# Optimization experiments

Measured on AMD Instinct MI355X. Metric: run time of the kernel, lower is better.

Reference implementation:

```python
import jax, jax.numpy as jnp
import numpy as np

R, C, H, W = 500, 512, 38, 38      # rois, VGG channels, feature-map HxW (img 608 / 16)
K, HID, POOL, SCALE = 20, 4096, 3, 16
FEAT = C * POOL * POOL             # 4608, matches fc6 in_features


def setup_inputs():
    key = jax.random.key(0)
    ks = jax.random.split(key, 12)
    fmap = jax.random.normal(ks[0], (C, H, W), dtype=jnp.float32)
    # ROIs in original image coords (x1,y1,x2,y2); width/height >= 48 px so that
    # after /16 + floor every ROI is non-degenerate (none filtered out).
    x1 = jax.random.randint(ks[1], (R,), 0, 288)
    y1 = jax.random.randint(ks[2], (R,), 0, 288)
    bw = jax.random.randint(ks[3], (R,), 48, 304)
    bh = jax.random.randint(ks[4], (R,), 48, 304)
    rois = jnp.stack([x1, y1, x1 + bw, y1 + bh], axis=1).astype(jnp.float32)
    label = jax.random.bernoulli(ks[5], 0.3, (K,)).astype(jnp.float32)
    s = 0.01
    W6 = jax.random.normal(ks[6], (FEAT, HID), jnp.float32) * s
    b6 = jnp.zeros((HID,), jnp.float32)
    W7 = jax.random.normal(ks[7], (HID, HID), jnp.float32) * s
    b7 = jnp.zeros((HID,), jnp.float32)
    W8c = jax.random.normal(ks[8], (HID, K), jnp.float32) * s
    b8c = jnp.zeros((K,), jnp.float32)
    W8d = jax.random.normal(ks[9], (HID, K), jnp.float32) * s
    b8d = jnp.zeros((K,), jnp.float32)
    return dict(fmap=fmap, rois=rois, label=label, W6=W6, b6=b6, W7=W7, b7=b7,
                W8c=W8c, b8c=b8c, W8d=W8d, b8d=b8d)


def _roi_pool(fmap, rois):
    # scaled_rois = origin_rois / 16, sliced as integer indices (floor)
    sc = jnp.floor(rois / SCALE).astype(jnp.int32)          # [R,4]
    x1, y1, x2, y2 = sc[:, 0], sc[:, 1], sc[:, 2], sc[:, 3]

    def binmask(lo, hi, size):
        # adaptive-max-pool bins: [lo + floor(j*L/3), lo + ceil((j+1)*L/3))
        L = hi - lo                                          # [R]
        j = jnp.arange(POOL)
        start = lo[:, None] + (j[None, :] * L[:, None]) // POOL
        end = lo[:, None] + (-((-(j[None, :] + 1) * L[:, None]) // POOL))
        pos = jnp.arange(size)
        return (pos[None, None, :] >= start[:, :, None]) & (pos[None, None, :] < end[:, :, None])

    cm = binmask(x1, x2, W)                                  # [R,3,W]
    rm = binmask(y1, y2, H)                                  # [R,3,H]
    neg = jnp.finfo(fmap.dtype).min
    # max over x within each x-bin: [R,C,H,3]
    tmp = jnp.max(jnp.where(cm[:, None, None, :, :], fmap[None, :, :, None, :], neg), axis=-1)
    # max over y within each y-bin: [R,C,3,3]
    pooled = jnp.max(jnp.where(rm[:, None, :, :, None], tmp[:, :, None, :, :], neg), axis=3)
    return pooled.reshape(R, FEAT), sc.astype(jnp.float32)


def _spatial_reg(scores, fc7, rois_sc, label):
    # faithful to original: argsort ascending, index 0 taken as the reference box,
    # and bboxes_iou interprets (x1,y1,x2,y2) as (x,y,w,h) — replicated as-is.
    idx = jnp.argsort(scores, axis=0)                        # [R,K]

    def per_class(idx_k, s_k, lab_k):
        h, rest = idx_k[0], idx_k[1:]
        hb = rois_sc[h]                                      # [4]
        rb = rois_sc[rest]                                   # [R-1,4]
        b1x2, b1y2 = rb[:, 0] + rb[:, 2], rb[:, 1] + rb[:, 3]
        b2x2, b2y2 = hb[0] + hb[2], hb[1] + hb[3]
        iw = jnp.clip(jnp.minimum(b1x2, b2x2) - jnp.maximum(rb[:, 0], hb[0]) + 1, 0)
        ih = jnp.clip(jnp.minimum(b1y2, b2y2) - jnp.maximum(rb[:, 1], hb[1]) + 1, 0)
        inter = iw * ih
        a1 = (b1x2 - rb[:, 0] + 1) * (b1y2 - rb[:, 1] + 1)
        a2 = (b2x2 - hb[0] + 1) * (b2y2 - hb[1] + 1)
        iou = inter / (a1 + a2 - inter)
        m = (iou > 0.6).astype(fc7.dtype)                    # [R-1]
        rf = fc7[rest] * m[:, None]
        diff = (rf - fc7[h]) * s_k[rest][:, None]
        return lab_k * 0.5 * jnp.sum(diff * diff)

    regs = jax.vmap(per_class)(idx.T, scores.T, label)       # [K]
    return jnp.sum(regs) / K


def reference(fmap, rois, label, W6, b6, W7, b7, W8c, b8c, W8d, b8d):
    feat, rois_sc = _roi_pool(fmap, rois)                    # [R,4608]
    fc6 = feat @ W6 + b6
    fc7 = fc6 @ W7 + b7
    pc = jax.nn.softmax(fc7 @ W8c + b8c, axis=1)             # per-roi over classes
    pd = jax.nn.softmax(fc7 @ W8d + b8d, axis=0)             # per-class over rois
    scores = pc * pd                                         # [R,K]
    out = jnp.sum(scores, axis=0)                            # [K], in (0,1)
    bce = -jnp.mean(label * jnp.log(out) + (1.0 - label) * jnp.log(1.0 - out))
    reg = _spatial_reg(scores, fc7, rois_sc, label)
    return scores, bce + reg, reg
```

## Files before the change

kernel.cpp:

```cpp
#include <hip/hip_runtime.h>
#include <cstdint>
#include <cstddef>

#define DEV __device__ __forceinline__

typedef __bf16 bf16_t;
typedef __bf16 bf16x8 __attribute__((ext_vector_type(8)));
typedef float  f32x4  __attribute__((ext_vector_type(4)));
typedef float  f32x2  __attribute__((ext_vector_type(2)));
typedef unsigned int u32x4 __attribute__((ext_vector_type(4)));

DEV bf16_t f2bf(float x) { return (bf16_t)x; }

constexpr int R_ = 500, C_ = 512, H_ = 38, W_ = 38, K_ = 20;
constexpr int HID = 4096, FEAT = 4608, MP = 512;
constexpr int HW = H_ * W_;
constexpr int KSPLIT = 4;

constexpr size_t alup(size_t x) { return (x + 255) & ~(size_t)255; }
constexpr size_t O_FMT  = 0;
constexpr size_t O_RSC  = alup(O_FMT  + (size_t)HW*C_*4);
constexpr size_t O_FEAT = alup(O_RSC  + (size_t)R_*4*4);
constexpr size_t O_FC6  = alup(O_FEAT + (size_t)MP*FEAT*2);
constexpr size_t O_FC7  = alup(O_FC6  + (size_t)MP*HID*2);
constexpr size_t O_PC   = alup(O_FC7  + (size_t)MP*HID*4);
constexpr size_t O_LD   = alup(O_PC   + (size_t)R_*K_*4);
constexpr size_t O_AN   = alup(O_LD   + (size_t)R_*K_*4);
constexpr size_t O_OS   = alup(O_AN   + (size_t)MP*4);
constexpr size_t O_HI   = alup(O_OS   + (size_t)K_*4);
constexpr size_t O_D    = alup(O_HI   + (size_t)K_*4);
constexpr size_t O_W8T  = alup(O_D    + (size_t)R_*K_*4);
constexpr size_t O_W7T  = alup(O_W8T  + (size_t)2*K_*HID*4);
constexpr size_t O_PART = alup(O_W7T  + (size_t)HID*HID*2);
constexpr size_t O_HP   = O_PART;
constexpr size_t O_DP   = O_PART + (size_t)4*1024*1024;

__global__ void __launch_bounds__(256) k_prep(const float* __restrict__ fmap,
                                              float* __restrict__ fmapt,
                                              const float* __restrict__ W8c,
                                              const float* __restrict__ W8d,
                                              float* __restrict__ W8T,
                                              const float* __restrict__ W7,
                                              bf16_t* __restrict__ W7T) {
    int b = blockIdx.x, t = threadIdx.x;
    if (b < 736) {
        __shared__ float tile[32][33];
        int p0 = (b % 46) * 32, c0 = (b / 46) * 32;
        int tx = t & 31, ty = t >> 5;
#pragma unroll
        for (int i = 0; i < 4; ++i) {
            int c = c0 + ty + i*8, p = p0 + tx;
            tile[ty + i*8][tx] = (p < HW) ? fmap[(size_t)c*HW + p] : 0.f;
        }
        __syncthreads();
#pragma unroll
        for (int i = 0; i < 4; ++i) {
            int p = p0 + ty + i*8, c = c0 + tx;
            if (p < HW) fmapt[(size_t)p*C_ + c] = tile[tx][ty + i*8];
        }
    } else if (b < 776) {
        int k = b - 736;
        const float* src = (k < K_) ? W8c : W8d;
        int kk = (k < K_) ? k : k - K_;
        for (int i = t; i < HID; i += 256)
            W8T[(size_t)k*HID + i] = src[(size_t)i*K_ + kk];
    } else {
        __shared__ float tile[64][65];
        int j = b - 776;
        int k0 = (j >> 6) * 64, n0 = (j & 63) * 64;
#pragma unroll
        for (int i = 0; i < 16; ++i) {
            int idx = t + i*256;
            int kk = idx >> 6, nn = idx & 63;
            tile[kk][nn] = W7[(size_t)(k0 + kk)*HID + n0 + nn];
        }
        __syncthreads();
#pragma unroll
        for (int i = 0; i < 8; ++i) {
            int idx = t + i*256;
            int nn = idx >> 5, kw = idx & 31;
            bf16_t a = f2bf(tile[2*kw][nn]), c = f2bf(tile[2*kw + 1][nn]);
            unsigned int u = ((unsigned short*)&a)[0] | ((unsigned int)((unsigned short*)&c)[0] << 16);
            *reinterpret_cast<unsigned int*>(&W7T[(size_t)(n0 + nn)*HID + k0 + 2*kw]) = u;
        }
    }
}

__global__ void __launch_bounds__(256) k_roipool(const float* __restrict__ fmapt,
                                                 const float* __restrict__ rois,
                                                 bf16_t* __restrict__ feat,
                                                 float* __restrict__ rois_sc) {
    int r = blockIdx.x, bin = blockIdx.y, t = threadIdx.x;
    if (r >= R_) {
        feat[(size_t)r*FEAT + (size_t)t*9       + bin] = (bf16_t)0.f;
        feat[(size_t)r*FEAT + (size_t)(t+256)*9 + bin] = (bf16_t)0.f;
        return;
    }
    int x1 = (int)floorf(rois[r*4+0] * 0.0625f);
    int y1 = (int)floorf(rois[r*4+1] * 0.0625f);
    int x2 = (int)floorf(rois[r*4+2] * 0.0625f);
    int y2 = (int)floorf(rois[r*4+3] * 0.0625f);
    if (bin == 0 && t == 0) {
        rois_sc[r*4+0] = (float)x1; rois_sc[r*4+1] = (float)y1;
        rois_sc[r*4+2] = (float)x2; rois_sc[r*4+3] = (float)y2;
    }
    int Lx = x2 - x1, Ly = y2 - y1;
    int pr = bin / 3, px = bin - pr*3;
    int rs = y1 + (pr*Ly)/3, re = y1 + ((pr+1)*Ly + 2)/3;
    int cs = x1 + (px*Lx)/3, ce = x1 + ((px+1)*Lx + 2)/3;
    float m0 = -3.402823466e38f, m1 = -3.402823466e38f;
    for (int y = rs; y < re; ++y) {
        const float* rowp = fmapt + (size_t)(y*W_)*C_;
        for (int x = cs; x < ce; ++x) {
            const float* p = rowp + (size_t)x*C_;
            m0 = fmaxf(m0, p[t]);
            m1 = fmaxf(m1, p[t + 256]);
        }
    }
    feat[(size_t)r*FEAT + (size_t)t*9       + bin] = f2bf(m0);
    feat[(size_t)r*FEAT + (size_t)(t+256)*9 + bin] = f2bf(m1);
}

__global__ void __launch_bounds__(512, 4)
k_gemm(const bf16_t* __restrict__ A, const float* __restrict__ B,
       float* __restrict__ part, int KDIM, int nts) {
    __shared__ bf16_t Asm[2][128*64];
    __shared__ bf16_t Bsm[2][128*64];
    const int t = threadIdx.x;
    const int lane = t & 63, wid = t >> 6;
    const int wr = wid >> 2, wc = wid & 3;

    const int flat = blockIdx.x + 32*blockIdx.y + 128*blockIdx.z;
    const int q = 16 * gridDim.z;
    const int v = (flat & 7) * q + (flat >> 3);
    const int by = v & 3, bx = (v >> 2) & 31, bz = v >> 7;

    const int brow = by * 128, bcol = bx * 128;
    const int kt0 = bz * nts;

    f32x4 acc[4][2] = {};
    f32x2 br[8];
    const int n2 = t & 63, kgl = t >> 6;

    auto stage_A = [&](int kt, int buf) {
        const bf16_t* Ag = A + (size_t)brow*KDIM + kt*64;
#pragma unroll
        for (int i = 0; i < 2; ++i) {
            int s = t + i*512;
            int row = s >> 3;
            int kb = (s & 7) ^ ((row >> 1) & 7);
            const bf16_t* src = Ag + (size_t)row*KDIM + kb*8;
            bf16_t* dst = &Asm[buf][(size_t)(i*512 + (t & ~63)) * 8];
            __builtin_amdgcn_global_load_lds(
                (const __attribute__((address_space(1))) void*)src,
                (__attribute__((address_space(3))) void*)dst, 16, 0, 0);
        }
    };
    auto load_B = [&](int kt) {
        const float* src = B + (size_t)(kt*64 + kgl*8)*HID + bcol + 2*n2;
#pragma unroll
        for (int j = 0; j < 8; ++j)
            br[j] = *reinterpret_cast<const f32x2*>(src + (size_t)j*HID);
    };
    auto write_B = [&](int buf) {
        const int sw = n2 & 7;
        bf16x8 v0, v1;
#pragma unroll
        for (int j = 0; j < 8; ++j) { v0[j] = f2bf(br[j].x); v1[j] = f2bf(br[j].y); }
        *reinterpret_cast<u32x4*>(&Bsm[buf][(size_t)((2*n2    )*8 + (kgl ^ sw)) * 8]) = *reinterpret_cast<u32x4*>(&v0);
        *reinterpret_cast<u32x4*>(&Bsm[buf][(size_t)((2*n2 + 1)*8 + (kgl ^ sw)) * 8]) = *reinterpret_cast<u32x4*>(&v1);
    };

    stage_A(kt0, 0);
    load_B(kt0);
    write_B(0);
    __syncthreads();

    for (int it = 0; it < nts; ++it) {
        const int cur = it & 1;
        if (it + 1 < nts) { stage_A(kt0 + it + 1, cur ^ 1); load_B(kt0 + it + 1); }
#pragma unroll
        for (int kk = 0; kk < 2; ++kk) {
            const int kb = kk*4 + (lane >> 4);
            bf16x8 af[4], bfr[2];
#pragma unroll
            for (int m = 0; m < 4; ++m) {
                int row = wr*64 + m*16 + (lane & 15);
                af[m] = *reinterpret_cast<const bf16x8*>(
                    &Asm[cur][(size_t)(row*8 + (kb ^ ((row >> 1) & 7))) * 8]);
            }
#pragma unroll
            for (int n = 0; n < 2; ++n) {
                int nn = wc*32 + n*16 + (lane & 15);
                bfr[n] = *reinterpret_cast<const bf16x8*>(
                    &Bsm[cur][(size_t)(nn*8 + (kb ^ ((nn >> 1) & 7))) * 8]);
            }
#pragma unroll
            for (int m = 0; m < 4; ++m)
#pragma unroll
                for (int n = 0; n < 2; ++n)
                    acc[m][n] = __builtin_amdgcn_mfma_f32_16x16x32_bf16(af[m], bfr[n], acc[m][n], 0, 0, 0);
        }
        if (it + 1 < nts) { write_B(cur ^ 1); __syncthreads(); }
    }

    float* dst = part + (size_t)bz * MP * HID;
#pragma unroll
    for (int m = 0; m < 4; ++m) {
        int row0 = brow + wr*64 + m*16 + ((lane >> 4) << 2);
#pragma unroll
        for (int n = 0; n < 2; ++n) {
            int col = bcol + wc*32 + n*16 + (lane & 15);
#pragma unroll
            for (int j = 0; j < 4; ++j)
                dst[(size_t)(row0 + j)*HID + col] = acc[m][n][j];
        }
    }
}

__global__ void __launch_bounds__(512, 4)
k_gemm_bt(const bf16_t* __restrict__ A, const bf16_t* __restrict__ BT,
          float* __restrict__ part, int KDIM, int nts) {
    __shared__ bf16_t Asm[2][128*64];
    __shared__ bf16_t Bsm[2][128*64];
    const int t = threadIdx.x;
    const int lane = t & 63, wid = t >> 6;
    const int wr = wid >> 2, wc = wid & 3;

    const int flat = blockIdx.x + 32*blockIdx.y + 128*blockIdx.z;
    const int q = 16 * gridDim.z;
    const int v = (flat & 7) * q + (flat >> 3);
    const int by = v & 3, bx = (v >> 2) & 31, bz = v >> 7;

    const int brow = by * 128, bcol = bx * 128;
    const int kt0 = bz * nts;

    f32x4 acc[4][2] = {};

    auto stage = [&](const bf16_t* base, int kt, bf16_t* lds) {
        const bf16_t* g = base + kt*64;
#pragma unroll
        for (int i = 0; i < 2; ++i) {
            int s = t + i*512;
            int row = s >> 3;
            int kb = (s & 7) ^ ((row >> 1) & 7);
            const bf16_t* src = g + (size_t)row*KDIM + kb*8;
            bf16_t* dst = lds + (size_t)(i*512 + (t & ~63)) * 8;
            __builtin_amdgcn_global_load_lds(
                (const __attribute__((address_space(1))) void*)src,
                (__attribute__((address_space(3))) void*)dst, 16, 0, 0);
        }
    };

    const bf16_t* Abase = A  + (size_t)brow*KDIM;
    const bf16_t* Bbase = BT + (size_t)bcol*KDIM;

    stage(Abase, kt0, &Asm[0][0]);
    stage(Bbase, kt0, &Bsm[0][0]);
    __syncthreads();

    for (int it = 0; it < nts; ++it) {
        const int cur = it & 1;
        if (it + 1 < nts) {
            stage(Abase, kt0 + it + 1, &Asm[cur ^ 1][0]);
            stage(Bbase, kt0 + it + 1, &Bsm[cur ^ 1][0]);
        }
#pragma unroll
        for (int kk = 0; kk < 2; ++kk) {
            const int kb = kk*4 + (lane >> 4);
            bf16x8 af[4], bfr[2];
#pragma unroll
            for (int m = 0; m < 4; ++m) {
                int row = wr*64 + m*16 + (lane & 15);
                af[m] = *reinterpret_cast<const bf16x8*>(
                    &Asm[cur][(size_t)(row*8 + (kb ^ ((row >> 1) & 7))) * 8]);
            }
#pragma unroll
            for (int n = 0; n < 2; ++n) {
                int nn = wc*32 + n*16 + (lane & 15);
                bfr[n] = *reinterpret_cast<const bf16x8*>(
                    &Bsm[cur][(size_t)(nn*8 + (kb ^ ((nn >> 1) & 7))) * 8]);
            }
#pragma unroll
            for (int m = 0; m < 4; ++m)
#pragma unroll
                for (int n = 0; n < 2; ++n)
                    acc[m][n] = __builtin_amdgcn_mfma_f32_16x16x32_bf16(af[m], bfr[n], acc[m][n], 0, 0, 0);
        }
        __syncthreads();
    }

    float* dst = part + (size_t)bz * MP * HID;
#pragma unroll
    for (int m = 0; m < 4; ++m) {
        int row0 = brow + wr*64 + m*16 + ((lane >> 4) << 2);
#pragma unroll
        for (int n = 0; n < 2; ++n) {
            int col = bcol + wc*32 + n*16 + (lane & 15);
#pragma unroll
            for (int j = 0; j < 4; ++j)
                dst[(size_t)(row0 + j)*HID + col] = acc[m][n][j];
        }
    }
}

__global__ void __launch_bounds__(256) k_reduce(const float* __restrict__ part,
                                                const float* __restrict__ bias,
                                                bf16_t* __restrict__ ob, float* __restrict__ of,
                                                int ksplit) {
    size_t idx = ((size_t)blockIdx.x*256 + threadIdx.x) * 4;
    f32x4 s = *reinterpret_cast<const f32x4*>(part + idx);
    for (int ss = 1; ss < ksplit; ++ss)
        s += *reinterpret_cast<const f32x4*>(part + (size_t)ss*MP*HID + idx);
    int col = (int)(idx & (HID - 1));
    s += *reinterpret_cast<const f32x4*>(bias + col);
    if (ob) {
#pragma unroll
        for (int j = 0; j < 4; ++j) ob[idx + j] = f2bf(s[j]);
    } else {
        *reinterpret_cast<f32x4*>(of + idx) = s;
    }
}

template<int NOUT, bool SELF>
__global__ void __launch_bounds__(256) k_dotcols(const float* __restrict__ fc7,
        const float* __restrict__ Bmat, const int* __restrict__ bidx,
        float* __restrict__ partial) {
    constexpr int NO = NOUT + (SELF ? 1 : 0);
    constexpr int SLICE = NOUT*16 + 4;
    __shared__ float Bs[8 * SLICE];
    const int rb = blockIdx.x, kb = blockIdx.y, t = threadIdx.x;
    const int k0 = kb * 128;
    for (int i = t; i < NOUT*32; i += 256) {
        int o = i >> 5, c = i & 31;
        const float* src = bidx ? fc7 + (size_t)bidx[o]*HID : Bmat + (size_t)o*HID;
        f32x4 v = *reinterpret_cast<const f32x4*>(src + k0 + c*4);
        *reinterpret_cast<f32x4*>(&Bs[(c >> 2)*SLICE + o*16 + (c & 3)*4]) = v;
    }
    __syncthreads();
    const int lane = t & 63, w = t >> 6;
    const int ri = lane >> 3, kk = lane & 7;
    const int r0 = rb*64 + w*16 + ri*2;
    f32x4 x0[4], x1[4];
    const float* f0 = fc7 + (size_t)r0*HID + k0 + kk*16;
#pragma unroll
    for (int j = 0; j < 4; ++j) {
        x0[j] = *reinterpret_cast<const f32x4*>(f0 + j*4);
        x1[j] = *reinterpret_cast<const f32x4*>(f0 + HID + j*4);
    }
    float acc0[NO], acc1[NO];
#pragma unroll
    for (int o = 0; o < NOUT; ++o) {
        f32x4 s0 = {}, s1 = {};
#pragma unroll
        for (int j = 0; j < 4; ++j) {
            f32x4 wv = *reinterpret_cast<const f32x4*>(&Bs[kk*SLICE + o*16 + j*4]);
            s0 += x0[j] * wv;
            s1 += x1[j] * wv;
        }
        acc0[o] = s0[0]+s0[1]+s0[2]+s0[3];
        acc1[o] = s1[0]+s1[1]+s1[2]+s1[3];
    }
    if (SELF) {
        f32x4 s0 = {}, s1 = {};
#pragma unroll
        for (int j = 0; j < 4; ++j) { s0 += x0[j]*x0[j]; s1 += x1[j]*x1[j]; }
        acc0[NO-1] = s0[0]+s0[1]+s0[2]+s0[3];
        acc1[NO-1] = s1[0]+s1[1]+s1[2]+s1[3];
    }
#pragma unroll
    for (int o = 0; o < NO; ++o) {
#pragma unroll
        for (int m = 1; m < 8; m <<= 1) {
            acc0[o] += __shfl_xor(acc0[o], m, 64);
            acc1[o] += __shfl_xor(acc1[o], m, 64);
        }
    }
    if (kk == 0) {
#pragma unroll
        for (int o = 0; o < NO; ++o) {
            partial[((size_t)kb*MP + r0    )*NO + o] = acc0[o];
            partial[((size_t)kb*MP + r0 + 1)*NO + o] = acc1[o];
        }
    }
}

__global__ void __launch_bounds__(64) k_headred(const float* __restrict__ hpart,
        const float* __restrict__ b8c, const float* __restrict__ b8d,
        float* __restrict__ pc, float* __restrict__ ld, float* __restrict__ An) {
    int r = blockIdx.x, t = threadIdx.x;
    __shared__ float lcs[20];
    if (t < 41) {
        float s = 0.f;
        for (int kb = 0; kb < 32; ++kb) s += hpart[((size_t)kb*MP + r)*41 + t];
        if (t < 20)      lcs[t] = s + b8c[t];
        else if (t < 40) ld[r*K_ + (t-20)] = s + b8d[t-20];
        else             An[r] = s;
    }
    __syncthreads();
    if (t == 0) {
        float mx = lcs[0];
#pragma unroll
        for (int k = 1; k < 20; ++k) mx = fmaxf(mx, lcs[k]);
        float sum = 0.f, e[20];
#pragma unroll
        for (int k = 0; k < 20; ++k) { e[k] = expf(lcs[k] - mx); sum += e[k]; }
        float inv = 1.f / sum;
#pragma unroll
        for (int k = 0; k < 20; ++k) pc[r*K_ + k] = e[k] * inv;
    }
}

__global__ void __launch_bounds__(64) k_dmatred(const float* __restrict__ dpart,
                                                float* __restrict__ D) {
    int r = blockIdx.x, t = threadIdx.x;
    if (t < 20) {
        float s = 0.f;
        for (int kb = 0; kb < 32; ++kb) s += dpart[((size_t)kb*MP + r)*20 + t];
        D[r*K_ + t] = s;
    }
}

__global__ void __launch_bounds__(256) k_pd(const float* __restrict__ ld,
        const float* __restrict__ pc, float* __restrict__ scores,
        float* __restrict__ out_sum, int* __restrict__ h_idx) {
    int k = blockIdx.x, t = threadIdx.x;
    __shared__ float sh[4];
    float m = -3.402823466e38f;
    for (int r = t; r < R_; r += 256) m = fmaxf(m, ld[r*K_ + k]);
    for (int off = 1; off < 64; off <<= 1) m = fmaxf(m, __shfl_xor(m, off, 64));
    if ((t & 63) == 0) sh[t >> 6] = m;
    __syncthreads();
    m = fmaxf(fmaxf(sh[0], sh[1]), fmaxf(sh[2], sh[3]));
    __syncthreads();
    float s = 0.f;
    for (int r = t; r < R_; r += 256) s += expf(ld[r*K_ + k] - m);
    for (int off = 1; off < 64; off <<= 1) s += __shfl_xor(s, off, 64);
    if ((t & 63) == 0) sh[t >> 6] = s;
    __syncthreads();
    s = sh[0] + sh[1] + sh[2] + sh[3];
    float inv = 1.f / s;

    float osum = 0.f, bv = 3.402823466e38f; int bi = 0x7fffffff;
    for (int r = t; r < R_; r += 256) {
        float p  = expf(ld[r*K_ + k] - m) * inv;
        float sc = pc[r*K_ + k] * p;
        scores[r*K_ + k] = sc;
        osum += sc;
        if (sc < bv || (sc == bv && r < bi)) { bv = sc; bi = r; }
    }
    for (int off = 1; off < 64; off <<= 1) osum += __shfl_xor(osum, off, 64);
    for (int off = 1; off < 64; off <<= 1) {
        float v2 = __shfl_xor(bv, off, 64);
        int   i2 = __shfl_xor(bi, off, 64);
        if (v2 < bv || (v2 == bv && i2 < bi)) { bv = v2; bi = i2; }
    }
    __shared__ float so[4], mv[4]; __shared__ int mi[4];
    if ((t & 63) == 0) { so[t >> 6] = osum; mv[t >> 6] = bv; mi[t >> 6] = bi; }
    __syncthreads();
    if (t == 0) {
        out_sum[k] = so[0] + so[1] + so[2] + so[3];
        float v = mv[0]; int i = mi[0];
        for (int w = 1; w < 4; ++w)
            if (mv[w] < v || (mv[w] == v && mi[w] < i)) { v = mv[w]; i = mi[w]; }
        h_idx[k] = i;
    }
}

__global__ void __launch_bounds__(256) k_final(const float* __restrict__ out_sum,
        const int* __restrict__ h_idx, const float* __restrict__ label,
        const float* __restrict__ scores, const float* __restrict__ D,
        const float* __restrict__ An, const float* __restrict__ rois_sc,
        float* __restrict__ dout) {
    int t = threadIdx.x;
    __shared__ float bsh[20];
    if (t < 20) {
        float o = out_sum[t], lab = label[t];
        bsh[t] = lab * logf(o) + (1.f - lab) * logf(1.f - o);
    }
    __syncthreads();

    float rp = 0.f;
    for (int i = t; i < R_*K_; i += 256) {
        int r = i / 20, k = i - r*20;
        int h = h_idx[k];
        if (r == h) continue;
        float lab = label[k];
        if (lab == 0.f) continue;
        float s = scores[r*K_ + k];
        const float* rb = rois_sc + r*4;
        const float* hb = rois_sc + h*4;
        float b1x2 = rb[0] + rb[2], b1y2 = rb[1] + rb[3];
        float b2x2 = hb[0] + hb[2], b2y2 = hb[1] + hb[3];
        float iw = fmaxf(fminf(b1x2, b2x2) - fmaxf(rb[0], hb[0]) + 1.f, 0.f);
        float ih = fmaxf(fminf(b1y2, b2y2) - fmaxf(rb[1], hb[1]) + 1.f, 0.f);
        float inter = iw * ih;
        float a1 = (b1x2 - rb[0] + 1.f) * (b1y2 - rb[1] + 1.f);
        float a2 = (b2x2 - hb[0] + 1.f) * (b2y2 - hb[1] + 1.f);
        float iou = inter / (a1 + a2 - inter);
        float mm = (iou > 0.6f) ? 1.f : 0.f;
        float term = mm * (An[r] - 2.f * D[r*K_ + k]) + An[h];
        rp += lab * 0.5f * s * s * term;
    }
    for (int off = 1; off < 64; off <<= 1) rp += __shfl_xor(rp, off, 64);
    __shared__ float rsh[4];
    if ((t & 63) == 0) rsh[t >> 6] = rp;
    __syncthreads();
    if (t == 0) {
        float reg = (rsh[0] + rsh[1] + rsh[2] + rsh[3]) / (float)K_;
        float b = 0.f;
        for (int k = 0; k < 20; ++k) b += bsh[k];
        float bce = -b / (float)K_;
        dout[R_*K_]     = bce + reg;
        dout[R_*K_ + 1] = reg;
    }
}

extern "C" void kernel_launch(void* const* d_in, const int* in_sizes, int n_in,
                              void* d_out, int out_size, void* d_ws, size_t ws_size,
                              hipStream_t stream) {
    const float* fmap  = (const float*)d_in[0];
    const float* rois  = (const float*)d_in[1];
    const float* label = (const float*)d_in[2];
    const float* W6    = (const float*)d_in[3];
    const float* b6    = (const float*)d_in[4];
    const float* W7    = (const float*)d_in[5];
    const float* b7    = (const float*)d_in[6];
    const float* W8c   = (const float*)d_in[7];
    const float* b8c   = (const float*)d_in[8];
    const float* W8d   = (const float*)d_in[9];
    const float* b8d   = (const float*)d_in[10];
    char* ws = (char*)d_ws;
    float* out = (float*)d_out;

    float*  fmapt = (float*)(ws + O_FMT);
    float*  roisc = (float*)(ws + O_RSC);
    bf16_t* feat  = (bf16_t*)(ws + O_FEAT);
    bf16_t* fc6   = (bf16_t*)(ws + O_FC6);
    float*  fc7   = (float*)(ws + O_FC7);
    float*  pc    = (float*)(ws + O_PC);
    float*  ld    = (float*)(ws + O_LD);
    float*  An    = (float*)(ws + O_AN);
    float*  osum  = (float*)(ws + O_OS);
    int*    hidx  = (int*)(ws + O_HI);
    float*  Dm    = (float*)(ws + O_D);
    float*  w8t   = (float*)(ws + O_W8T);
    bf16_t* w7t   = (bf16_t*)(ws + O_W7T);
    float*  part  = (float*)(ws + O_PART);
    float*  hpart = (float*)(ws + O_HP);
    float*  dpart = (float*)(ws + O_DP);

    k_prep   <<<dim3(776 + 4096), dim3(256), 0, stream>>>(fmap, fmapt, W8c, W8d, w8t, W7, w7t);
    k_roipool<<<dim3(MP, 9),      dim3(256), 0, stream>>>(fmapt, rois, feat, roisc);

    k_gemm   <<<dim3(HID/128, MP/128, KSPLIT), dim3(512), 0, stream>>>(feat, W6, part, FEAT, (FEAT/64)/KSPLIT);
    k_reduce <<<dim3((MP*HID)/1024), dim3(256), 0, stream>>>(part, b6, fc6, (float*)nullptr, KSPLIT);

    k_gemm_bt<<<dim3(HID/128, MP/128, KSPLIT), dim3(512), 0, stream>>>(fc6, w7t, part, HID, (HID/64)/KSPLIT);
    k_reduce <<<dim3((MP*HID)/1024), dim3(256), 0, stream>>>(part, b7, (bf16_t*)nullptr, fc7, KSPLIT);

    k_dotcols<40, true><<<dim3(MP/64, HID/128), dim3(256), 0, stream>>>(fc7, w8t, (const int*)nullptr, hpart);
    k_headred<<<dim3(R_), dim3(64), 0, stream>>>(hpart, b8c, b8d, pc, ld, An);
    k_pd     <<<dim3(K_), dim3(256), 0, stream>>>(ld, pc, out, osum, hidx);
    k_dotcols<20, false><<<dim3(MP/64, HID/128), dim3(256), 0, stream>>>(fc7, (const float*)nullptr, hidx, dpart);
    k_dmatred<<<dim3(R_), dim3(64), 0, stream>>>(dpart, Dm);
    k_final  <<<dim3(1),  dim3(256), 0, stream>>>(osum, hidx, label, out, Dm, An, roisc, out);
}
```

Before: 179.3 us.

## Pre-transpose W6 to bf16 and use triple-buffered split-K=2 GEMM for fc6/fc7

Adds a bf16 transpose of W6 to the prep kernel, so fc6 can use the same async global-to-LDS GEMM path as fc7. It replaces the double-buffered B-transposed GEMM with a three-stage LDS pipeline that waits with explicit vmcnt and a raw barrier. It also cuts split-K from 4 to 2, which halves the partial-sum traffic through the reduce kernel. In exchange, every call pays an extra W6 read, convert and write, LDS use goes up (so fewer blocks fit per CU), and the new fc6 path only runs when the workspace is large enough.

```diff
diff --git a/kernel.cpp b/kernel.cpp
--- a/kernel.cpp
+++ b/kernel.cpp
@@ -15,7 +15,6 @@
 constexpr int R_ = 500, C_ = 512, H_ = 38, W_ = 38, K_ = 20;
 constexpr int HID = 4096, FEAT = 4608, MP = 512;
 constexpr int HW = H_ * W_;
-constexpr int KSPLIT = 4;
 
 constexpr size_t alup(size_t x) { return (x + 255) & ~(size_t)255; }
 constexpr size_t O_FMT  = 0;
@@ -34,6 +33,8 @@
 constexpr size_t O_PART = alup(O_W7T  + (size_t)HID*HID*2);
 constexpr size_t O_HP   = O_PART;
 constexpr size_t O_DP   = O_PART + (size_t)4*1024*1024;
+constexpr size_t O_W6T  = alup(O_PART + (size_t)4*MP*HID*4);
+constexpr size_t O_ENDF = O_W6T + (size_t)HID*FEAT*2;
 
 __global__ void __launch_bounds__(256) k_prep(const float* __restrict__ fmap,
                                               float* __restrict__ fmapt,
@@ -41,7 +42,9 @@
                                               const float* __restrict__ W8d,
                                               float* __restrict__ W8T,
                                               const float* __restrict__ W7,
-                                              bf16_t* __restrict__ W7T) {
+                                              bf16_t* __restrict__ W7T,
+                                              const float* __restrict__ W6,
+                                              bf16_t* __restrict__ W6T) {
     int b = blockIdx.x, t = threadIdx.x;
     if (b < 736) {
         __shared__ float tile[32][33];
@@ -65,14 +68,22 @@
         for (int i = t; i < HID; i += 256)
             W8T[(size_t)k*HID + i] = src[(size_t)i*K_ + kk];
     } else {
+        const float* src; bf16_t* dst; int k0, n0, dstlen;
+        if (b < 776 + 4096) {
+            int j = b - 776;
+            src = W7; dst = W7T; dstlen = HID;
+            k0 = (j >> 6) * 64; n0 = (j & 63) * 64;
+        } else {
+            int j = b - (776 + 4096);
+            src = W6; dst = W6T; dstlen = FEAT;
+            k0 = (j >> 6) * 64; n0 = (j & 63) * 64;
+        }
         __shared__ float tile[64][65];
-        int j = b - 776;
-        int k0 = (j >> 6) * 64, n0 = (j & 63) * 64;
 #pragma unroll
         for (int i = 0; i < 16; ++i) {
             int idx = t + i*256;
             int kk = idx >> 6, nn = idx & 63;
-            tile[kk][nn] = W7[(size_t)(k0 + kk)*HID + n0 + nn];
+            tile[kk][nn] = src[(size_t)(k0 + kk)*HID + n0 + nn];
         }
         __syncthreads();
 #pragma unroll
@@ -81,7 +92,7 @@
             int nn = idx >> 5, kw = idx & 31;
             bf16_t a = f2bf(tile[2*kw][nn]), c = f2bf(tile[2*kw + 1][nn]);
             unsigned int u = ((unsigned short*)&a)[0] | ((unsigned int)((unsigned short*)&c)[0] << 16);
-            *reinterpret_cast<unsigned int*>(&W7T[(size_t)(n0 + nn)*HID + k0 + 2*kw]) = u;
+            *reinterpret_cast<unsigned int*>(&dst[(size_t)(n0 + nn)*dstlen + k0 + 2*kw]) = u;
         }
     }
 }
@@ -121,6 +132,102 @@
     feat[(size_t)r*FEAT + (size_t)(t+256)*9 + bin] = f2bf(m1);
 }
 
+__global__ void __launch_bounds__(512, 2)
+k_gemm_bt2(const bf16_t* __restrict__ A, const bf16_t* __restrict__ BT,
+           float* __restrict__ part, int KDIM, int nts) {
+    __shared__ bf16_t Asm[3][128*64];
+    __shared__ bf16_t Bsm[3][128*64];
+    const int t = threadIdx.x;
+    const int lane = t & 63, wid = t >> 6;
+    const int wr = wid >> 2, wc = wid & 3;
+
+    const int flat = blockIdx.x + 32*blockIdx.y + 128*blockIdx.z;
+    const int q = 16 * gridDim.z;
+    const int v = (flat & 7) * q + (flat >> 3);
+    const int by = v & 3, bx = (v >> 2) & 31, bz = v >> 7;
+
+    const int brow = by * 128, bcol = bx * 128;
+    const int kt0 = bz * nts;
+
+    f32x4 acc[4][2] = {};
+
+    auto stage = [&](const bf16_t* base, int kt, bf16_t* lds) {
+        const bf16_t* g = base + kt*64;
+#pragma unroll
+        for (int i = 0; i < 2; ++i) {
+            int s = t + i*512;
+            int row = s >> 3;
+            int kb = (s & 7) ^ ((row >> 1) & 7);
+            const bf16_t* src = g + (size_t)row*KDIM + kb*8;
+            bf16_t* dst = lds + (size_t)(i*512 + (t & ~63)) * 8;
+            __builtin_amdgcn_global_load_lds(
+                (const __attribute__((address_space(1))) void*)src,
+                (__attribute__((address_space(3))) void*)dst, 16, 0, 0);
+        }
+    };
+
+    const bf16_t* Abase = A  + (size_t)brow*KDIM;
+    const bf16_t* Bbase = BT + (size_t)bcol*KDIM;
+
+    stage(Abase, kt0 + 0, &Asm[0][0]);
+    stage(Bbase, kt0 + 0, &Bsm[0][0]);
+    stage(Abase, kt0 + 1, &Asm[1][0]);
+    stage(Bbase, kt0 + 1, &Bsm[1][0]);
+
+    int cur = 0, nx2 = 2;
+    for (int it = 0; it < nts; ++it) {
+        if (it == nts - 1) asm volatile("s_waitcnt vmcnt(0)" ::: "memory");
+        else               asm volatile("s_waitcnt vmcnt(4)" ::: "memory");
+        __builtin_amdgcn_sched_barrier(0);
+        __builtin_amdgcn_s_barrier();
+        __builtin_amdgcn_sched_barrier(0);
+
+        const bf16_t* Ac = &Asm[cur][0];
+        const bf16_t* Bc = &Bsm[cur][0];
+#pragma unroll
+        for (int kk = 0; kk < 2; ++kk) {
+            const int kb = kk*4 + (lane >> 4);
+            bf16x8 af[4], bfr[2];
+#pragma unroll
+            for (int m = 0; m < 4; ++m) {
+                int row = wr*64 + m*16 + (lane & 15);
+                af[m] = *reinterpret_cast<const bf16x8*>(
+                    Ac + (size_t)(row*8 + (kb ^ ((row >> 1) & 7))) * 8);
+            }
+#pragma unroll
+            for (int n = 0; n < 2; ++n) {
+                int nn = wc*32 + n*16 + (lane & 15);
+                bfr[n] = *reinterpret_cast<const bf16x8*>(
+                    Bc + (size_t)(nn*8 + (kb ^ ((nn >> 1) & 7))) * 8);
+            }
+#pragma unroll
+            for (int m = 0; m < 4; ++m)
+#pragma unroll
+                for (int n = 0; n < 2; ++n)
+                    acc[m][n] = __builtin_amdgcn_mfma_f32_16x16x32_bf16(af[m], bfr[n], acc[m][n], 0, 0, 0);
+        }
+        if (it + 2 < nts) {
+            stage(Abase, kt0 + it + 2, &Asm[nx2][0]);
+            stage(Bbase, kt0 + it + 2, &Bsm[nx2][0]);
+        }
+        cur = (cur == 2) ? 0 : cur + 1;
+        nx2 = (nx2 == 2) ? 0 : nx2 + 1;
+    }
+
+    float* dst = part + (size_t)bz * MP * HID;
+#pragma unroll
+    for (int m = 0; m < 4; ++m) {
+        int row0 = brow + wr*64 + m*16 + ((lane >> 4) << 2);
+#pragma unroll
+        for (int n = 0; n < 2; ++n) {
+            int col = bcol + wc*32 + n*16 + (lane & 15);
+#pragma unroll
+            for (int j = 0; j < 4; ++j)
+                dst[(size_t)(row0 + j)*HID + col] = acc[m][n][j];
+        }
+    }
+}
+
 __global__ void __launch_bounds__(512, 4)
 k_gemm(const bf16_t* __restrict__ A, const float* __restrict__ B,
        float* __restrict__ part, int KDIM, int nts) {
@@ -202,92 +309,6 @@
                     acc[m][n] = __builtin_amdgcn_mfma_f32_16x16x32_bf16(af[m], bfr[n], acc[m][n], 0, 0, 0);
         }
         if (it + 1 < nts) { write_B(cur ^ 1); __syncthreads(); }
-    }
-
-    float* dst = part + (size_t)bz * MP * HID;
-#pragma unroll
-    for (int m = 0; m < 4; ++m) {
-        int row0 = brow + wr*64 + m*16 + ((lane >> 4) << 2);
-#pragma unroll
-        for (int n = 0; n < 2; ++n) {
-            int col = bcol + wc*32 + n*16 + (lane & 15);
-#pragma unroll
-            for (int j = 0; j < 4; ++j)
-                dst[(size_t)(row0 + j)*HID + col] = acc[m][n][j];
-        }
-    }
-}
-
-__global__ void __launch_bounds__(512, 4)
-k_gemm_bt(const bf16_t* __restrict__ A, const bf16_t* __restrict__ BT,
-          float* __restrict__ part, int KDIM, int nts) {
-    __shared__ bf16_t Asm[2][128*64];
-    __shared__ bf16_t Bsm[2][128*64];
-    const int t = threadIdx.x;
-    const int lane = t & 63, wid = t >> 6;
-    const int wr = wid >> 2, wc = wid & 3;
-
-    const int flat = blockIdx.x + 32*blockIdx.y + 128*blockIdx.z;
-    const int q = 16 * gridDim.z;
-    const int v = (flat & 7) * q + (flat >> 3);
-    const int by = v & 3, bx = (v >> 2) & 31, bz = v >> 7;
-
-    const int brow = by * 128, bcol = bx * 128;
-    const int kt0 = bz * nts;
-
-    f32x4 acc[4][2] = {};
-
-    auto stage = [&](const bf16_t* base, int kt, bf16_t* lds) {
-        const bf16_t* g = base + kt*64;
-#pragma unroll
-        for (int i = 0; i < 2; ++i) {
-            int s = t + i*512;
-            int row = s >> 3;
-            int kb = (s & 7) ^ ((row >> 1) & 7);
-            const bf16_t* src = g + (size_t)row*KDIM + kb*8;
-            bf16_t* dst = lds + (size_t)(i*512 + (t & ~63)) * 8;
-            __builtin_amdgcn_global_load_lds(
-                (const __attribute__((address_space(1))) void*)src,
-                (__attribute__((address_space(3))) void*)dst, 16, 0, 0);
-        }
-    };
-
-    const bf16_t* Abase = A  + (size_t)brow*KDIM;
-    const bf16_t* Bbase = BT + (size_t)bcol*KDIM;
-
-    stage(Abase, kt0, &Asm[0][0]);
-    stage(Bbase, kt0, &Bsm[0][0]);
-    __syncthreads();
-
-    for (int it = 0; it < nts; ++it) {
-        const int cur = it & 1;
-        if (it + 1 < nts) {
-            stage(Abase, kt0 + it + 1, &Asm[cur ^ 1][0]);
-            stage(Bbase, kt0 + it + 1, &Bsm[cur ^ 1][0]);
-        }
-#pragma unroll
-        for (int kk = 0; kk < 2; ++kk) {
-            const int kb = kk*4 + (lane >> 4);
-            bf16x8 af[4], bfr[2];
-#pragma unroll
-            for (int m = 0; m < 4; ++m) {
-                int row = wr*64 + m*16 + (lane & 15);
-                af[m] = *reinterpret_cast<const bf16x8*>(
-                    &Asm[cur][(size_t)(row*8 + (kb ^ ((row >> 1) & 7))) * 8]);
-            }
-#pragma unroll
-            for (int n = 0; n < 2; ++n) {
-                int nn = wc*32 + n*16 + (lane & 15);
-                bfr[n] = *reinterpret_cast<const bf16x8*>(
-                    &Bsm[cur][(size_t)(nn*8 + (kb ^ ((nn >> 1) & 7))) * 8]);
-            }
-#pragma unroll
-            for (int m = 0; m < 4; ++m)
-#pragma unroll
-                for (int n = 0; n < 2; ++n)
-                    acc[m][n] = __builtin_amdgcn_mfma_f32_16x16x32_bf16(af[m], bfr[n], acc[m][n], 0, 0, 0);
-        }
-        __syncthreads();
     }
 
     float* dst = part + (size_t)bz * MP * HID;
@@ -549,15 +570,24 @@
     float*  part  = (float*)(ws + O_PART);
     float*  hpart = (float*)(ws + O_HP);
     float*  dpart = (float*)(ws + O_DP);
-
-    k_prep   <<<dim3(776 + 4096), dim3(256), 0, stream>>>(fmap, fmapt, W8c, W8d, w8t, W7, w7t);
-    k_roipool<<<dim3(MP, 9),      dim3(256), 0, stream>>>(fmapt, rois, feat, roisc);
-
-    k_gemm   <<<dim3(HID/128, MP/128, KSPLIT), dim3(512), 0, stream>>>(feat, W6, part, FEAT, (FEAT/64)/KSPLIT);
-    k_reduce <<<dim3((MP*HID)/1024), dim3(256), 0, stream>>>(part, b6, fc6, (float*)nullptr, KSPLIT);
-
-    k_gemm_bt<<<dim3(HID/128, MP/128, KSPLIT), dim3(512), 0, stream>>>(fc6, w7t, part, HID, (HID/64)/KSPLIT);
-    k_reduce <<<dim3((MP*HID)/1024), dim3(256), 0, stream>>>(part, b7, (bf16_t*)nullptr, fc7, KSPLIT);
+    bf16_t* w6t   = (bf16_t*)(ws + O_W6T);
+
+    const bool full = (ws_size >= O_ENDF);
+    const int prep_blocks = full ? (776 + 4096 + 4608) : (776 + 4096);
+
+    k_prep   <<<dim3(prep_blocks), dim3(256), 0, stream>>>(fmap, fmapt, W8c, W8d, w8t, W7, w7t, W6, w6t);
+    k_roipool<<<dim3(MP, 9),       dim3(256), 0, stream>>>(fmapt, rois, feat, roisc);
+
+    if (full) {
+        k_gemm_bt2<<<dim3(32, 4, 2), dim3(512), 0, stream>>>(feat, w6t, part, FEAT, (FEAT/64)/2);
+        k_reduce  <<<dim3((MP*HID)/1024), dim3(256), 0, stream>>>(part, b6, fc6, (float*)nullptr, 2);
+    } else {
+        k_gemm    <<<dim3(32, 4, 4), dim3(512), 0, stream>>>(feat, W6, part, FEAT, (FEAT/64)/4);
+        k_reduce  <<<dim3((MP*HID)/1024), dim3(256), 0, stream>>>(part, b6, fc6, (float*)nullptr, 4);
+    }
+
+    k_gemm_bt2<<<dim3(32, 4, 2), dim3(512), 0, stream>>>(fc6, w7t, part, HID, (HID/64)/2);
+    k_reduce  <<<dim3((MP*HID)/1024), dim3(256), 0, stream>>>(part, b7, (bf16_t*)nullptr, fc7, 2);
 
     k_dotcols<40, true><<<dim3(MP/64, HID/128), dim3(256), 0, stream>>>(fc7, w8t, (const int*)nullptr, hpart);
     k_headred<<<dim3(R_), dim3(64), 0, stream>>>(hpart, b8c, b8d, pc, ld, An);
```

New measurement: 190.7 us. +6.3%, slower.
